# Optimization experiments

Hardware: AMD Instinct MI355X
Metric: run time of the kernel (lower is better)

The kernel has to match this reference:

```python
import jax, jax.numpy as jnp
import numpy as np

B, IN, H = 16384, 512, 512


def setup_inputs() -> dict:
    key = jax.random.key(0)
    ks = jax.random.split(key, 7)
    s_in = 1.0 / np.sqrt(IN)
    s_h = 1.0 / np.sqrt(H)
    return {
        "x": jax.random.normal(ks[0], (B, IN), jnp.float32),
        "h": jax.random.normal(ks[1], (B, H), jnp.float32),
        "c": jax.random.normal(ks[2], (B, H), jnp.float32),
        # packed gate weights, order [i, f, g, o] along last dim (4*H)
        "Wx": jax.random.normal(ks[3], (IN, 4 * H), jnp.float32) * s_in,
        "Wh": jax.random.normal(ks[4], (H, 4 * H), jnp.float32) * s_h,
        "bx": jax.random.normal(ks[5], (4 * H,), jnp.float32) * s_in,
        "bh": jax.random.normal(ks[6], (4 * H,), jnp.float32) * s_h,
    }


def reference(x, h, c, Wx, Wh, bx, bh):
    # one fused GEMM per input stream instead of 8 small linears; same math
    gates = x @ Wx + bx + h @ Wh + bh          # [B, 4H]
    gi, gf, gg, go = jnp.split(gates, 4, axis=-1)
    i = jax.nn.sigmoid(gi)
    f = jax.nn.sigmoid(gf)
    g = jnp.tanh(gg)
    o = jax.nn.sigmoid(go)
    c_new = f * c + i * g
    h_new = o * jnp.tanh(c_new)
    return (h_new, c_new)
```

## Files before the change

kernel.cpp:

```cpp
#include <hip/hip_runtime.h>
#include <hip/hip_bf16.h>

#define B_DIM   16384
#define IN_DIM  512
#define H_DIM   512
#define K_DIM   1024
#define N4H     2048
#define BH      (B_DIM * H_DIM)

typedef __attribute__((ext_vector_type(8))) short  short8;
typedef __attribute__((ext_vector_type(4))) short  short4v;
typedef __attribute__((ext_vector_type(4))) float  f32x4;

__device__ inline void async_load16(const void* g, void* l) {
    __builtin_amdgcn_global_load_lds(
        (const __attribute__((address_space(1))) void*)g,
        (__attribute__((address_space(3)))       void*)l, 16, 0, 0);
}

__device__ inline short bf16bits(float f) {
    __hip_bfloat16 b = __float2bfloat16(f);
    return *reinterpret_cast<short*>(&b);
}

__device__ inline float sigmoidf_(float v) {
    return 1.0f / (1.0f + __expf(-v));
}
__device__ inline float tanhf_(float v) {
    v = fminf(fmaxf(v, -30.f), 30.f);
    float e = __expf(2.f * v);
    return (e - 1.f) / (e + 1.f);
}

__global__ __launch_bounds__(256) void prep_all(
    const float* __restrict__ Wx, const float* __restrict__ Wh,
    const float* __restrict__ bx, const float* __restrict__ bh,
    const float* __restrict__ x,  const float* __restrict__ h,
    __hip_bfloat16* __restrict__ Wt, __hip_bfloat16* __restrict__ Axh,
    float* __restrict__ bias_p) {
    const int bid = blockIdx.x;
    const int t   = threadIdx.x;

    if (bid < 2048) {
        __shared__ __hip_bfloat16 tile[32][33];
        const int bk = bid & 31;
        const int bn = bid >> 5;
        const int kb = bk * 32, nb = bn * 32;
#pragma unroll
        for (int r = 0; r < 4; ++r) {
            int k_loc = r * 8 + (t >> 5);
            int n_loc = t & 31;
            int kg = kb + k_loc;
            float v = (kg < IN_DIM) ? Wx[(size_t)kg * N4H + nb + n_loc]
                                    : Wh[(size_t)(kg - IN_DIM) * N4H + nb + n_loc];
            tile[k_loc][n_loc] = __float2bfloat16(v);
        }
        __syncthreads();
        {
            int n_loc = t >> 3;
            int k_loc = (t & 7) * 4;
            int ng = nb + n_loc;
            int g  = ng >> 9;
            int c  = ng & 511;
            int row_out = (c >> 5) * 128 + g * 32 + (c & 31);
            short4v v4;
            v4.x = *reinterpret_cast<short*>(&tile[k_loc + 0][n_loc]);
            v4.y = *reinterpret_cast<short*>(&tile[k_loc + 1][n_loc]);
            v4.z = *reinterpret_cast<short*>(&tile[k_loc + 2][n_loc]);
            v4.w = *reinterpret_cast<short*>(&tile[k_loc + 3][n_loc]);
            *(short4v*)&Wt[(size_t)row_out * K_DIM + kb + k_loc] = v4;
        }
        if (bid < 8) {
            int ng = bid * 256 + t;
            int g  = ng >> 9;
            int c  = ng & 511;
            int ro = (c >> 5) * 128 + g * 32 + (c & 31);
            bias_p[ro] = bx[ng] + bh[ng];
        }
    } else {
        const int ab = bid - 2048;
        const int kq = t;
        const float* src = (kq < 128) ? (x + kq * 4)
                                      : (h + (size_t)(kq - 128) * 4);
#pragma unroll
        for (int j = 0; j < 8; ++j) {
            int m = ab * 8 + j;
            float4 v = *(const float4*)(src + (size_t)m * 512);
            short4v sv;
            sv.x = bf16bits(v.x);
            sv.y = bf16bits(v.y);
            sv.z = bf16bits(v.z);
            sv.w = bf16bits(v.w);
            *(short4v*)&Axh[(size_t)m * K_DIM + kq * 4] = sv;
        }
    }
}

__global__ __launch_bounds__(256, 3) void lstm_gemm(
    const float* __restrict__ c_in,
    const __hip_bfloat16* __restrict__ Axh,
    const __hip_bfloat16* __restrict__ Wt,
    const float* __restrict__ bias_p,
    float* __restrict__ out) {
    __shared__ __hip_bfloat16 lds_a[2][128 * 32];
    __shared__ __hip_bfloat16 lds_b[2][128 * 32];

    const int tid   = threadIdx.x;
    const int w     = tid >> 6;
    const int lane  = tid & 63;
    const int col16 = lane & 15;
    const int quad  = lane >> 4;

    const int jb    = blockIdx.x;
    const int xcd   = jb & 7;
    const int local = jb >> 3;
    const int bm    = xcd * 16 + (local >> 4);
    const int bn    = local & 15;

    f32x4 acc[2][8];
#pragma unroll
    for (int mi = 0; mi < 2; ++mi)
#pragma unroll
        for (int ni = 0; ni < 8; ++ni)
            acc[mi][ni] = (f32x4){0.f, 0.f, 0.f, 0.f};

    const __hip_bfloat16* Ab = Axh + (size_t)bm * 128 * K_DIM;
    const __hip_bfloat16* Bb = Wt  + (size_t)bn * 128 * K_DIM;

    const int s0 = w * 128 + lane;
    const int s1 = s0 + 64;
    const int r0 = s0 >> 2, r1 = s1 >> 2;
    const int q0 = ((s0 & 3) - ((r0 >> 1) & 3)) & 3;
    const int q1 = ((s1 & 3) - ((r1 >> 1) & 3)) & 3;
    const size_t ga0 = (size_t)r0 * K_DIM + q0 * 8;
    const size_t ga1 = (size_t)r1 * K_DIM + q1 * 8;

    int aoff[2], boff[8];
#pragma unroll
    for (int mi = 0; mi < 2; ++mi) {
        int r = w * 32 + mi * 16 + col16;
        aoff[mi] = (r * 4 + ((quad + ((r >> 1) & 3)) & 3)) * 16;
    }
#pragma unroll
    for (int ni = 0; ni < 8; ++ni) {
        int r = ni * 16 + col16;
        boff[ni] = (r * 4 + ((quad + ((r >> 1) & 3)) & 3)) * 16;
    }

    async_load16(Ab + ga0, (void*)(&lds_a[0][w * 1024]));
    async_load16(Ab + ga1, (void*)(&lds_a[0][w * 1024 + 512]));
    async_load16(Bb + ga0, (void*)(&lds_b[0][w * 1024]));
    async_load16(Bb + ga1, (void*)(&lds_b[0][w * 1024 + 512]));

    for (int kt = 0; kt < 32; ++kt) {
        __syncthreads();
        const int p = kt & 1;
        if (kt < 31) {
            const int kb = (kt + 1) * 32;
            async_load16(Ab + ga0 + kb, (void*)(&lds_a[1 - p][w * 1024]));
            async_load16(Ab + ga1 + kb, (void*)(&lds_a[1 - p][w * 1024 + 512]));
            async_load16(Bb + ga0 + kb, (void*)(&lds_b[1 - p][w * 1024]));
            async_load16(Bb + ga1 + kb, (void*)(&lds_b[1 - p][w * 1024 + 512]));
        }
        const char* lap = (const char*)lds_a[p];
        const char* lbp = (const char*)lds_b[p];

        short8 afr[2], bfr[8];
#pragma unroll
        for (int mi = 0; mi < 2; ++mi)
            afr[mi] = *(const short8*)(lap + aoff[mi]);
#pragma unroll
        for (int ni = 0; ni < 8; ++ni)
            bfr[ni] = *(const short8*)(lbp + boff[ni]);
#pragma unroll
        for (int mi = 0; mi < 2; ++mi)
#pragma unroll
            for (int ni = 0; ni < 8; ++ni)
                acc[mi][ni] = __builtin_amdgcn_mfma_f32_16x16x32_bf16(
                    afr[mi], bfr[ni], acc[mi][ni], 0, 0, 0);
    }

    float bias_v[4][2];
#pragma unroll
    for (int g = 0; g < 4; ++g)
#pragma unroll
        for (int h2 = 0; h2 < 2; ++h2)
            bias_v[g][h2] = bias_p[bn * 128 + g * 32 + h2 * 16 + col16];

#pragma unroll
    for (int mi = 0; mi < 2; ++mi) {
#pragma unroll
        for (int reg = 0; reg < 4; ++reg) {
            const int m_g = bm * 128 + w * 32 + mi * 16 + quad * 4 + reg;
#pragma unroll
            for (int h2 = 0; h2 < 2; ++h2) {
                const int hc_g = bn * 32 + h2 * 16 + col16;
                float gi = acc[mi][0 + h2][reg] + bias_v[0][h2];
                float gf = acc[mi][2 + h2][reg] + bias_v[1][h2];
                float gg = acc[mi][4 + h2][reg] + bias_v[2][h2];
                float go = acc[mi][6 + h2][reg] + bias_v[3][h2];
                float iv = sigmoidf_(gi);
                float fv = sigmoidf_(gf);
                float gv = tanhf_(gg);
                float ov = sigmoidf_(go);
                float co = c_in[(size_t)m_g * H_DIM + hc_g];
                float cn = fv * co + iv * gv;
                float hn = ov * tanhf_(cn);
                out[(size_t)m_g * H_DIM + hc_g]      = hn;
                out[BH + (size_t)m_g * H_DIM + hc_g] = cn;
            }
        }
    }
}

__global__ __launch_bounds__(256) void prep_weights_fb(
    const float* __restrict__ Wx, const float* __restrict__ Wh,
    const float* __restrict__ bx, const float* __restrict__ bh,
    __hip_bfloat16* __restrict__ Wt, float* __restrict__ bias_p) {
    __shared__ __hip_bfloat16 tile[32][33];
    const int bid = blockIdx.x;
    const int bk  = bid & 31;
    const int bn  = bid >> 5;
    const int t   = threadIdx.x;
    const int kb  = bk * 32, nb = bn * 32;
#pragma unroll
    for (int r = 0; r < 4; ++r) {
        int k_loc = r * 8 + (t >> 5);
        int n_loc = t & 31;
        int kg = kb + k_loc;
        float v = (kg < IN_DIM) ? Wx[(size_t)kg * N4H + nb + n_loc]
                                : Wh[(size_t)(kg - IN_DIM) * N4H + nb + n_loc];
        tile[k_loc][n_loc] = __float2bfloat16(v);
    }
    __syncthreads();
    {
        int n_loc = t >> 3;
        int k_loc = (t & 7) * 4;
        int ng = nb + n_loc;
        int g  = ng >> 9;
        int c  = ng & 511;
        int row_out = (c >> 5) * 128 + g * 32 + (c & 31);
        short4v v4;
        v4.x = *reinterpret_cast<short*>(&tile[k_loc + 0][n_loc]);
        v4.y = *reinterpret_cast<short*>(&tile[k_loc + 1][n_loc]);
        v4.z = *reinterpret_cast<short*>(&tile[k_loc + 2][n_loc]);
        v4.w = *reinterpret_cast<short*>(&tile[k_loc + 3][n_loc]);
        *(short4v*)&Wt[(size_t)row_out * K_DIM + kb + k_loc] = v4;
    }
    if (bid < 8) {
        int ng = bid * 256 + t;
        int g  = ng >> 9;
        int c  = ng & 511;
        int ro = (c >> 5) * 128 + g * 32 + (c & 31);
        bias_p[ro] = bx[ng] + bh[ng];
    }
}

__global__ __launch_bounds__(256, 3) void lstm_gemm_fb(
    const float* __restrict__ x, const float* __restrict__ h,
    const float* __restrict__ c_in,
    const __hip_bfloat16* __restrict__ Wt, const float* __restrict__ bias_p,
    float* __restrict__ out) {
    __shared__ __hip_bfloat16 lds_a[128 * 32];
    __shared__ __hip_bfloat16 lds_b[128 * 32];
    const int tid   = threadIdx.x;
    const int bn    = blockIdx.x & 15;
    const int bm    = blockIdx.x >> 4;
    const int w     = tid >> 6;
    const int lane  = tid & 63;
    const int col16 = lane & 15;
    const int quad  = lane >> 4;
    f32x4 acc[2][8];
#pragma unroll
    for (int mi = 0; mi < 2; ++mi)
#pragma unroll
        for (int ni = 0; ni < 8; ++ni)
            acc[mi][ni] = (f32x4){0.f, 0.f, 0.f, 0.f};
    const __hip_bfloat16* wt_base = Wt + (size_t)(bn * 128) * K_DIM;
    const int chunk0 = w * 2;
    const int e0     = chunk0 * 512 + lane * 8;
    const int bn_loc0 = e0 >> 5, bk_off0 = e0 & 31;
    const int e1     = (chunk0 + 1) * 512 + lane * 8;
    const int bn_loc1 = e1 >> 5, bk_off1 = e1 & 31;
    for (int kt = 0; kt < 32; ++kt) {
        const int kb = kt * 32;
        const float* aptr;
        int koff;
        if (kb < IN_DIM) { aptr = x; koff = kb; }
        else             { aptr = h; koff = kb - IN_DIM; }
        async_load16(wt_base + (size_t)bn_loc0 * K_DIM + kb + bk_off0,
                     (void*)(lds_b + chunk0 * 512));
        async_load16(wt_base + (size_t)bn_loc1 * K_DIM + kb + bk_off1,
                     (void*)(lds_b + (chunk0 + 1) * 512));
        float4 av[4];
#pragma unroll
        for (int j = 0; j < 4; ++j) {
            int cch = j * 256 + tid;
            int row = cch >> 3;
            int kq  = (cch & 7) * 4;
            av[j] = *(const float4*)(aptr + (size_t)(bm * 128 + row) * IN_DIM
                                     + koff + kq);
        }
#pragma unroll
        for (int j = 0; j < 4; ++j) {
            int cch = j * 256 + tid;
            int row = cch >> 3;
            int kq  = (cch & 7) * 4;
            short4v sv;
            sv.x = bf16bits(av[j].x);
            sv.y = bf16bits(av[j].y);
            sv.z = bf16bits(av[j].z);
            sv.w = bf16bits(av[j].w);
            *(short4v*)&lds_a[row * 32 + kq] = sv;
        }
        __syncthreads();
        short8 afr[2], bfr[8];
#pragma unroll
        for (int mi = 0; mi < 2; ++mi)
            afr[mi] = *(const short8*)&lds_a[(w * 32 + mi * 16 + col16) * 32 + quad * 8];
#pragma unroll
        for (int ni = 0; ni < 8; ++ni)
            bfr[ni] = *(const short8*)&lds_b[(ni * 16 + col16) * 32 + quad * 8];
#pragma unroll
        for (int mi = 0; mi < 2; ++mi)
#pragma unroll
            for (int ni = 0; ni < 8; ++ni)
                acc[mi][ni] = __builtin_amdgcn_mfma_f32_16x16x32_bf16(
                    afr[mi], bfr[ni], acc[mi][ni], 0, 0, 0);
        __syncthreads();
    }
    float bias_v[4][2];
#pragma unroll
    for (int g = 0; g < 4; ++g)
#pragma unroll
        for (int h2 = 0; h2 < 2; ++h2)
            bias_v[g][h2] = bias_p[bn * 128 + g * 32 + h2 * 16 + col16];
#pragma unroll
    for (int mi = 0; mi < 2; ++mi) {
#pragma unroll
        for (int reg = 0; reg < 4; ++reg) {
            const int m_g = bm * 128 + w * 32 + mi * 16 + quad * 4 + reg;
#pragma unroll
            for (int h2 = 0; h2 < 2; ++h2) {
                const int hc_g = bn * 32 + h2 * 16 + col16;
                float gi = acc[mi][0 + h2][reg] + bias_v[0][h2];
                float gf = acc[mi][2 + h2][reg] + bias_v[1][h2];
                float gg = acc[mi][4 + h2][reg] + bias_v[2][h2];
                float go = acc[mi][6 + h2][reg] + bias_v[3][h2];
                float iv = sigmoidf_(gi);
                float fv = sigmoidf_(gf);
                float gv = tanhf_(gg);
                float ov = sigmoidf_(go);
                float co = c_in[(size_t)m_g * H_DIM + hc_g];
                float cn = fv * co + iv * gv;
                float hn = ov * tanhf_(cn);
                out[(size_t)m_g * H_DIM + hc_g]      = hn;
                out[BH + (size_t)m_g * H_DIM + hc_g] = cn;
            }
        }
    }
}

extern "C" void kernel_launch(void* const* d_in, const int* in_sizes, int n_in,
                              void* d_out, int out_size, void* d_ws, size_t ws_size,
                              hipStream_t stream) {
    const float* x  = (const float*)d_in[0];
    const float* h  = (const float*)d_in[1];
    const float* c  = (const float*)d_in[2];
    const float* Wx = (const float*)d_in[3];
    const float* Wh = (const float*)d_in[4];
    const float* bx = (const float*)d_in[5];
    const float* bh = (const float*)d_in[6];

    const size_t wtBytes  = (size_t)N4H * K_DIM * 2;
    const size_t axhBytes = (size_t)B_DIM * K_DIM * 2;
    const size_t need     = wtBytes + axhBytes + (size_t)N4H * 4;

    if (ws_size >= need) {
        __hip_bfloat16* Wt  = (__hip_bfloat16*)d_ws;
        __hip_bfloat16* Axh = (__hip_bfloat16*)((char*)d_ws + wtBytes);
        float* bias_p = (float*)((char*)d_ws + wtBytes + axhBytes);
        prep_all<<<4096, 256, 0, stream>>>(Wx, Wh, bx, bh, x, h, Wt, Axh, bias_p);
        lstm_gemm<<<2048, 256, 0, stream>>>(c, Axh, Wt, bias_p, (float*)d_out);
    } else {
        __hip_bfloat16* Wt = (__hip_bfloat16*)d_ws;
        float* bias_p = (float*)((char*)d_ws + wtBytes);
        prep_weights_fb<<<2048, 256, 0, stream>>>(Wx, Wh, bx, bh, Wt, bias_p);
        lstm_gemm_fb<<<2048, 256, 0, stream>>>(x, h, c, Wt, bias_p, (float*)d_out);
    }
}
```

Measured before the change: 249.1 us.

## Use 2x2 warp tiling in LSTM GEMM with LDS exchange of gate accumulators

Changes each wavefront's output tile from 32x128 to 64x64 (2x2 wave grid), so each k-step loads 4 A and 4 B fragments instead of 2 and 8, cutting LDS fragment reads per MFMA. Because the g/o gates now live in a different wave than i/f, the epilogue stages g and o pre-activations (with bias) into a swizzled LDS buffer reused from the operand buffers. Half the waves then compute the full LSTM cell update. This adds two barriers and leaves half the waves idle in the epilogue.

```diff
diff --git a/kernel.cpp b/kernel.cpp
--- a/kernel.cpp
+++ b/kernel.cpp
@@ -102,14 +102,15 @@
     const __hip_bfloat16* __restrict__ Wt,
     const float* __restrict__ bias_p,
     float* __restrict__ out) {
-    __shared__ __hip_bfloat16 lds_a[2][128 * 32];
-    __shared__ __hip_bfloat16 lds_b[2][128 * 32];
+    __shared__ __align__(16) unsigned char smem[32768];
 
     const int tid   = threadIdx.x;
     const int w     = tid >> 6;
     const int lane  = tid & 63;
     const int col16 = lane & 15;
     const int quad  = lane >> 4;
+    const int wm    = w >> 1;
+    const int wn    = w & 1;
 
     const int jb    = blockIdx.x;
     const int xcd   = jb & 7;
@@ -117,11 +118,11 @@
     const int bm    = xcd * 16 + (local >> 4);
     const int bn    = local & 15;
 
-    f32x4 acc[2][8];
-#pragma unroll
-    for (int mi = 0; mi < 2; ++mi)
-#pragma unroll
-        for (int ni = 0; ni < 8; ++ni)
+    f32x4 acc[4][4];
+#pragma unroll
+    for (int mi = 0; mi < 4; ++mi)
+#pragma unroll
+        for (int ni = 0; ni < 4; ++ni)
             acc[mi][ni] = (f32x4){0.f, 0.f, 0.f, 0.f};
 
     const __hip_bfloat16* Ab = Axh + (size_t)bm * 128 * K_DIM;
@@ -135,81 +136,113 @@
     const size_t ga0 = (size_t)r0 * K_DIM + q0 * 8;
     const size_t ga1 = (size_t)r1 * K_DIM + q1 * 8;
 
-    int aoff[2], boff[8];
-#pragma unroll
-    for (int mi = 0; mi < 2; ++mi) {
-        int r = w * 32 + mi * 16 + col16;
+    int aoff[4], boff[4];
+#pragma unroll
+    for (int mi = 0; mi < 4; ++mi) {
+        int r = wm * 64 + mi * 16 + col16;
         aoff[mi] = (r * 4 + ((quad + ((r >> 1) & 3)) & 3)) * 16;
     }
 #pragma unroll
-    for (int ni = 0; ni < 8; ++ni) {
-        int r = ni * 16 + col16;
+    for (int ni = 0; ni < 4; ++ni) {
+        int r = wn * 64 + ni * 16 + col16;
         boff[ni] = (r * 4 + ((quad + ((r >> 1) & 3)) & 3)) * 16;
     }
 
-    async_load16(Ab + ga0, (void*)(&lds_a[0][w * 1024]));
-    async_load16(Ab + ga1, (void*)(&lds_a[0][w * 1024 + 512]));
-    async_load16(Bb + ga0, (void*)(&lds_b[0][w * 1024]));
-    async_load16(Bb + ga1, (void*)(&lds_b[0][w * 1024 + 512]));
+    char* sbase = (char*)smem;
+
+    async_load16(Ab + ga0, sbase + w * 2048);
+    async_load16(Ab + ga1, sbase + w * 2048 + 1024);
+    async_load16(Bb + ga0, sbase + 8192 + w * 2048);
+    async_load16(Bb + ga1, sbase + 8192 + w * 2048 + 1024);
 
     for (int kt = 0; kt < 32; ++kt) {
         __syncthreads();
         const int p = kt & 1;
         if (kt < 31) {
             const int kb = (kt + 1) * 32;
-            async_load16(Ab + ga0 + kb, (void*)(&lds_a[1 - p][w * 1024]));
-            async_load16(Ab + ga1 + kb, (void*)(&lds_a[1 - p][w * 1024 + 512]));
-            async_load16(Bb + ga0 + kb, (void*)(&lds_b[1 - p][w * 1024]));
-            async_load16(Bb + ga1 + kb, (void*)(&lds_b[1 - p][w * 1024 + 512]));
-        }
-        const char* lap = (const char*)lds_a[p];
-        const char* lbp = (const char*)lds_b[p];
-
-        short8 afr[2], bfr[8];
-#pragma unroll
-        for (int mi = 0; mi < 2; ++mi)
+            char* nb_ = sbase + (1 - p) * 16384;
+            async_load16(Ab + ga0 + kb, nb_ + w * 2048);
+            async_load16(Ab + ga1 + kb, nb_ + w * 2048 + 1024);
+            async_load16(Bb + ga0 + kb, nb_ + 8192 + w * 2048);
+            async_load16(Bb + ga1 + kb, nb_ + 8192 + w * 2048 + 1024);
+        }
+        const char* lap = sbase + p * 16384;
+        const char* lbp = lap + 8192;
+
+        short8 afr[4], bfr[4];
+#pragma unroll
+        for (int mi = 0; mi < 4; ++mi)
             afr[mi] = *(const short8*)(lap + aoff[mi]);
 #pragma unroll
-        for (int ni = 0; ni < 8; ++ni)
+        for (int ni = 0; ni < 4; ++ni)
             bfr[ni] = *(const short8*)(lbp + boff[ni]);
 #pragma unroll
-        for (int mi = 0; mi < 2; ++mi)
-#pragma unroll
-            for (int ni = 0; ni < 8; ++ni)
+        for (int mi = 0; mi < 4; ++mi)
+#pragma unroll
+            for (int ni = 0; ni < 4; ++ni)
                 acc[mi][ni] = __builtin_amdgcn_mfma_f32_16x16x32_bf16(
                     afr[mi], bfr[ni], acc[mi][ni], 0, 0, 0);
     }
 
-    float bias_v[4][2];
-#pragma unroll
-    for (int g = 0; g < 4; ++g)
-#pragma unroll
-        for (int h2 = 0; h2 < 2; ++h2)
-            bias_v[g][h2] = bias_p[bn * 128 + g * 32 + h2 * 16 + col16];
-
-#pragma unroll
-    for (int mi = 0; mi < 2; ++mi) {
-#pragma unroll
-        for (int reg = 0; reg < 4; ++reg) {
-            const int m_g = bm * 128 + w * 32 + mi * 16 + quad * 4 + reg;
-#pragma unroll
-            for (int h2 = 0; h2 < 2; ++h2) {
-                const int hc_g = bn * 32 + h2 * 16 + col16;
-                float gi = acc[mi][0 + h2][reg] + bias_v[0][h2];
-                float gf = acc[mi][2 + h2][reg] + bias_v[1][h2];
-                float gg = acc[mi][4 + h2][reg] + bias_v[2][h2];
-                float go = acc[mi][6 + h2][reg] + bias_v[3][h2];
-                float iv = sigmoidf_(gi);
-                float fv = sigmoidf_(gf);
-                float gv = tanhf_(gg);
-                float ov = sigmoidf_(go);
-                float co = c_in[(size_t)m_g * H_DIM + hc_g];
-                float cn = fv * co + iv * gv;
-                float hn = ov * tanhf_(cn);
-                out[(size_t)m_g * H_DIM + hc_g]      = hn;
-                out[BH + (size_t)m_g * H_DIM + hc_g] = cn;
+    __syncthreads();
+    float* fx = (float*)smem;
+
+    if (wn == 1) {
+        float bg[2][2];
+#pragma unroll
+        for (int g2 = 0; g2 < 2; ++g2)
+#pragma unroll
+            for (int hh = 0; hh < 2; ++hh)
+                bg[g2][hh] = bias_p[bn * 128 + (2 + g2) * 32 + hh * 16 + col16];
+#pragma unroll
+        for (int mi = 0; mi < 4; ++mi)
+#pragma unroll
+            for (int ni = 0; ni < 4; ++ni) {
+                int g2 = ni >> 1, hh = ni & 1;
+                int hc = hh * 16 + col16;
+#pragma unroll
+                for (int reg = 0; reg < 4; ++reg) {
+                    int row = wm * 64 + mi * 16 + quad * 4 + reg;
+                    int sw = (hc + ((row >> 2) & 3) * 8) & 31;
+                    fx[g2 * 4096 + row * 32 + sw] = acc[mi][ni][reg] + bg[g2][hh];
+                }
             }
-        }
+    }
+    __syncthreads();
+    if (wn == 0) {
+        float bi[2][2];
+#pragma unroll
+        for (int g = 0; g < 2; ++g)
+#pragma unroll
+            for (int hh = 0; hh < 2; ++hh)
+                bi[g][hh] = bias_p[bn * 128 + g * 32 + hh * 16 + col16];
+#pragma unroll
+        for (int mi = 0; mi < 4; ++mi)
+#pragma unroll
+            for (int reg = 0; reg < 4; ++reg) {
+                int row = wm * 64 + mi * 16 + quad * 4 + reg;
+                size_t m_g = (size_t)(bm * 128 + row);
+                int swb = ((row >> 2) & 3) * 8;
+#pragma unroll
+                for (int hh = 0; hh < 2; ++hh) {
+                    int hc = hh * 16 + col16;
+                    int sw = (hc + swb) & 31;
+                    float gi = acc[mi][0 + hh][reg] + bi[0][hh];
+                    float gf = acc[mi][2 + hh][reg] + bi[1][hh];
+                    float gg = fx[row * 32 + sw];
+                    float go = fx[4096 + row * 32 + sw];
+                    float iv = sigmoidf_(gi);
+                    float fv = sigmoidf_(gf);
+                    float gv = tanhf_(gg);
+                    float ov = sigmoidf_(go);
+                    int col = bn * 32 + hc;
+                    float co = c_in[m_g * H_DIM + col];
+                    float cn = fv * co + iv * gv;
+                    float hn = ov * tanhf_(cn);
+                    out[m_g * H_DIM + col]      = hn;
+                    out[BH + m_g * H_DIM + col] = cn;
+                }
+            }
     }
 }
 
```

After: 253.7 us. No clear change (+1.9%).
